# Kernel tuning notes

Hardware: AMD Instinct MI355X
Metric: run time of the kernel (lower is better)

The kernel has to match this reference:

```python
import jax, jax.numpy as jnp
import numpy as np

B, Te, Td, D_ENC, D_DEC, ATT = 8, 512, 128, 512, 512, 256


def setup_inputs() -> dict:
    key = jax.random.key(0)
    k0, k1, k2, k3, k4 = jax.random.split(key, 5)
    return {
        "values": jax.random.normal(k0, (B, Te, D_ENC), dtype=jnp.float32),
        "query": jax.random.normal(k1, (B, Td, D_DEC), dtype=jnp.float32),
        "W_h": jax.random.uniform(k2, (D_ENC, ATT), jnp.float32, -0.05, 0.05),
        "U_a": jax.random.uniform(k3, (D_DEC, ATT), jnp.float32, -0.05, 0.05),
        "V_a": jax.random.uniform(k4, (1, ATT), jnp.float32, -0.05, 0.05),
    }


def reference(values, query, W_h, U_a, V_a):
    # values: [B, Te, D_ENC] encoder output sequence (single entry in 'values' list)
    # query:  [B, Td, D_DEC] decoder output sequence
    # With a single encoder sequence, broadcast_sum/broadcast_concat reduces are identities.
    W_hi = jnp.einsum('bse,ea->bsa', values, W_h)        # [B, Te, ATT]
    U_a_dot_s = jnp.einsum('btd,da->bta', query, U_a)    # [B, Td, ATT]
    # tanh(h.Wa + s.Ua): vectorized over all decoder timesteps (K.rnn scan unrolled)
    act = jnp.tanh(W_hi[:, None, :, :] + U_a_dot_s[:, :, None, :])  # [B, Td, Te, ATT]
    scores = jnp.einsum('btsa,a->bts', act, V_a[0])      # [B, Td, Te]
    e_outputs = jax.nn.softmax(scores, axis=-1)          # softmax over encoder positions
    # context: weighted sum of encoder hidden states
    c_outputs = jnp.einsum('bts,bse->bte', e_outputs, values)  # [B, Td, D_ENC]
    return (c_outputs, e_outputs)
```

## Files before the change

kernel.cpp:

```cpp
#include <hip/hip_runtime.h>
#include <hip/hip_bf16.h>


typedef __attribute__((ext_vector_type(8))) short bf16x8;
typedef __attribute__((ext_vector_type(4))) float f32x4;

__device__ inline void f32_to_bf16_pair(float x, short& h, short& l) {
    unsigned u = __builtin_bit_cast(unsigned, x);
    unsigned r = u + 0x7FFFu + ((u >> 16) & 1u);
    h = (short)(r >> 16);
    float xh = __builtin_bit_cast(float, r & 0xFFFF0000u);
    float xl = x - xh;
    unsigned u2 = __builtin_bit_cast(unsigned, xl);
    unsigned r2 = u2 + 0x7FFFu + ((u2 >> 16) & 1u);
    l = (short)(r2 >> 16);
}

__global__ __launch_bounds__(256) void prep(
    const float* __restrict__ W_h, const float* __restrict__ U_a,
    const float* __restrict__ values, const float* __restrict__ query,
    short* __restrict__ BHi, short* __restrict__ BLo,
    short* __restrict__ AHi, short* __restrict__ ALo)
{
    __shared__ float TW[64][65];
    __shared__ float TA[16][516];
    const int bid = blockIdx.x;
    const int tid = threadIdx.x;

    if (bid < 64) {
        const int mat = bid >> 5, nb = (bid >> 3) & 3, kb = bid & 7;
        const float* W = mat ? U_a : W_h;
        {
            const int krow = tid >> 2, cq = (tid & 3) * 16;
            const float* src = W + (size_t)(kb * 64 + krow) * 256 + nb * 64 + cq;
            #pragma unroll
            for (int q = 0; q < 4; ++q)
                *(float4*)&TW[krow][cq + q * 4] = *(const float4*)&src[q * 4];
        }
        __syncthreads();
        {
            const int f = tid >> 5;
            const int ngl = f >> 1, ksl = f & 1;
            const int l0 = (tid & 31) * 2;
            const int ngrp = nb * 4 + ngl;
            const int ksg = kb * 2 + ksl;
            const size_t base = (size_t)mat * 131072 + (size_t)(ngrp * 16 + ksg) * 512;
            #pragma unroll
            for (int li = 0; li < 2; ++li) {
                const int lane = l0 + li;
                const int lr = lane & 15, lg = lane >> 4;
                bf16x8 hv, lv;
                #pragma unroll
                for (int j = 0; j < 8; ++j) {
                    short h, l;
                    f32_to_bf16_pair(TW[ksl * 32 + lg * 8 + j][ngl * 16 + lr], h, l);
                    hv[j] = h; lv[j] = l;
                }
                *(bf16x8*)(BHi + base + lane * 8) = hv;
                *(bf16x8*)(BLo + base + lane * 8) = lv;
            }
        }
    } else {
        const int mg = bid - 64;
        const float* src = (mg < 256) ? values + (size_t)mg * 16 * 512
                                      : query + (size_t)(mg - 256) * 16 * 512;
        {
            const int row = tid >> 4, c0 = (tid & 15) * 4;
            #pragma unroll
            for (int i = 0; i < 8; ++i)
                *(float4*)&TA[row][c0 + i * 64] =
                    *(const float4*)&src[(size_t)row * 512 + c0 + i * 64];
        }
        __syncthreads();
        {
            const int ks = tid >> 4;
            const int l4 = (tid & 15) * 4;
            const size_t base = ((size_t)(mg * 16 + ks)) * 512;
            #pragma unroll
            for (int li = 0; li < 4; ++li) {
                const int lane = l4 + li;
                const int lr = lane & 15, lg = lane >> 4;
                bf16x8 hv, lv;
                #pragma unroll
                for (int j = 0; j < 8; ++j) {
                    short h, l;
                    f32_to_bf16_pair(TA[lr][ks * 32 + lg * 8 + j], h, l);
                    hv[j] = h; lv[j] = l;
                }
                *(bf16x8*)(AHi + base + lane * 8) = hv;
                *(bf16x8*)(ALo + base + lane * 8) = lv;
            }
        }
    }
}

__global__ __launch_bounds__(128) void gemm_mfma(
    const short* __restrict__ AHi, const short* __restrict__ ALo,
    const short* __restrict__ BHi, const short* __restrict__ BLo,
    float* __restrict__ EwO, float* __restrict__ EuO)
{
    const int bid = blockIdx.x;
    const int mt = bid >> 2, nt = bid & 3;
    const int tid = threadIdx.x;
    const int w = tid >> 6, l = tid & 63;
    const int lr = l & 15, lg = l >> 4;

    float* C; int m0, mg, matoff;
    if (mt < 128) { C = EwO; m0 = mt * 32; mg = mt * 2 + w; matoff = 0; }
    else { C = EuO; m0 = (mt - 128) * 32; mg = 256 + (mt - 128) * 2 + w; matoff = 131072; }

    const short* ah_p = AHi + ((size_t)mg * 16) * 512 + l * 8;
    const short* al_p = ALo + ((size_t)mg * 16) * 512 + l * 8;
    const short* bh_p = BHi + matoff + ((size_t)(nt * 4) * 16) * 512 + l * 8;
    const short* bl_p = BLo + matoff + ((size_t)(nt * 4) * 16) * 512 + l * 8;

    f32x4 acc[4];
    #pragma unroll
    for (int nc = 0; nc < 4; ++nc) acc[nc] = (f32x4){0.f, 0.f, 0.f, 0.f};

    #pragma unroll 2
    for (int ks = 0; ks < 16; ++ks) {
        bf16x8 ah = *(const bf16x8*)(ah_p + (size_t)ks * 512);
        bf16x8 al = *(const bf16x8*)(al_p + (size_t)ks * 512);
        #pragma unroll
        for (int nc = 0; nc < 4; ++nc) {
            bf16x8 bh = *(const bf16x8*)(bh_p + ((size_t)(nc * 16 + ks)) * 512);
            bf16x8 bl = *(const bf16x8*)(bl_p + ((size_t)(nc * 16 + ks)) * 512);
            acc[nc] = __builtin_amdgcn_mfma_f32_16x16x32_bf16(ah, bh, acc[nc], 0, 0, 0);
            acc[nc] = __builtin_amdgcn_mfma_f32_16x16x32_bf16(al, bh, acc[nc], 0, 0, 0);
            acc[nc] = __builtin_amdgcn_mfma_f32_16x16x32_bf16(ah, bl, acc[nc], 0, 0, 0);
        }
    }

    const float SCL = 2.8853900817779268f;
    float* cp = C + (size_t)(m0 + w * 16 + lg * 4) * 256 + nt * 64 + lr;
    #pragma unroll
    for (int nc = 0; nc < 4; ++nc)
        #pragma unroll
        for (int r = 0; r < 4; ++r)
            cp[(size_t)r * 256 + nc * 16] = __builtin_amdgcn_exp2f(acc[nc][r] * SCL);
}

__global__ __launch_bounds__(256) void scores_k(
    const float* __restrict__ Ew, const float* __restrict__ Eu,
    const float* __restrict__ Va, float* __restrict__ scoresP)
{
    __shared__ float Ws[64][68];
    __shared__ float Us[16][68];

    const int bid = blockIdx.x;
    const int b = bid & 7;
    const int rest = bid >> 3;
    const int ah = rest & 3;
    const int tt = (rest >> 2) & 7;
    const int st = rest >> 5;
    const int t0 = tt * 16, s0 = st * 64, a0 = ah * 64;
    const int tid = threadIdx.x;

    const int r = tid >> 2, c16 = (tid & 3) * 16;
    const float* wsrc = Ew + (size_t)(b * 512 + s0 + r) * 256 + a0 + c16;
    #pragma unroll
    for (int q = 0; q < 4; ++q)
        *(float4*)&Ws[r][c16 + q * 4] = *(const float4*)&wsrc[q * 4];
    const int r8 = tid >> 4, c8 = (tid & 15) * 4;
    const float* usrc = Eu + (size_t)(b * 128 + t0 + r8) * 256 + a0 + c8;
    *(float4*)&Us[r8][c8] = *(const float4*)&usrc[0];
    __syncthreads();

    const int t = tid >> 4;
    const int ss = tid & 15;
    const float* Vp = Va + a0;

    float acc[4] = {};
    #pragma unroll 4
    for (int a = 0; a < 64; a += 4) {
        float4 u  = *(const float4*)&Us[t][a];
        float4 w0 = *(const float4*)&Ws[ss][a];
        float4 w1 = *(const float4*)&Ws[ss + 16][a];
        float4 w2 = *(const float4*)&Ws[ss + 32][a];
        float4 w3 = *(const float4*)&Ws[ss + 48][a];
        const float uv[4] = {u.x, u.y, u.z, u.w};
        const float wv[4][4] = {{w0.x, w0.y, w0.z, w0.w}, {w1.x, w1.y, w1.z, w1.w},
                                {w2.x, w2.y, w2.z, w2.w}, {w3.x, w3.y, w3.z, w3.w}};
        #pragma unroll
        for (int q = 0; q < 4; ++q) {
            const float vq = Vp[a + q];
            #pragma unroll
            for (int k = 0; k < 4; ++k) {
                float e = wv[k][q] * uv[q];
                float rc = __builtin_amdgcn_rcpf(1.f + e);
                acc[k] = fmaf(vq, rc, acc[k]);
            }
        }
    }

    float* sp = scoresP + (size_t)ah * 524288
              + (size_t)(b * 128 + t0 + t) * 512 + s0 + ss;
    #pragma unroll
    for (int k = 0; k < 4; ++k) sp[k * 16] = acc[k];
}

__global__ __launch_bounds__(256) void softctx(
    const float* __restrict__ scoresP, const float* __restrict__ values,
    float* __restrict__ out_c, float* __restrict__ out_e)
{
    __shared__ float Ps[4][512];
    __shared__ float Part[7][4][128];

    const int bid = blockIdx.x;
    const int b = bid & 7;
    const int rest = bid >> 3;
    const int tg = rest & 31;
    const int eh = rest >> 5;
    const int t0 = tg * 4;
    const int tid = threadIdx.x;

    {
        const int row = tid >> 6, lane = tid & 63;
        const float* sp = scoresP + (size_t)(b * 128 + t0 + row) * 512;
        float e[8]; float ssum = 0.f;
        #pragma unroll
        for (int k = 0; k < 8; ++k) {
            const int idx = k * 64 + lane;
            float s = sp[idx] + sp[524288 + idx] + sp[1048576 + idx] + sp[1572864 + idx];
            e[k] = __builtin_amdgcn_exp2f(s * -2.8853900817779268f);
            ssum += e[k];
        }
        #pragma unroll
        for (int off = 32; off > 0; off >>= 1)
            ssum += __shfl_xor(ssum, off);
        const float inv = 1.0f / ssum;
        float* erow = out_e + (size_t)(b * 128 + t0 + row) * 512;
        #pragma unroll
        for (int k = 0; k < 8; ++k) {
            float p = e[k] * inv;
            Ps[row][k * 64 + lane] = p;
            if (eh == 0) erow[k * 64 + lane] = p;
        }
    }
    __syncthreads();

    const int sh = tid >> 5;
    const int el = (tid & 31) * 4;
    const int e4 = eh * 128 + el;
    const int sb = sh * 64;
    const float* vb = values + (size_t)b * 262144;

    float4 a0 = {0,0,0,0}, a1 = {0,0,0,0}, a2 = {0,0,0,0}, a3 = {0,0,0,0};
    #pragma unroll 2
    for (int s2 = 0; s2 < 64; s2 += 4) {
        float4 q0 = *(const float4*)&Ps[0][sb + s2];
        float4 q1 = *(const float4*)&Ps[1][sb + s2];
        float4 q2 = *(const float4*)&Ps[2][sb + s2];
        float4 q3 = *(const float4*)&Ps[3][sb + s2];
        const float q0v[4] = {q0.x, q0.y, q0.z, q0.w};
        const float q1v[4] = {q1.x, q1.y, q1.z, q1.w};
        const float q2v[4] = {q2.x, q2.y, q2.z, q2.w};
        const float q3v[4] = {q3.x, q3.y, q3.z, q3.w};
        #pragma unroll
        for (int j = 0; j < 4; ++j) {
            float4 v4 = *(const float4*)&vb[(size_t)(sb + s2 + j) * 512 + e4];
            a0.x = fmaf(q0v[j], v4.x, a0.x); a0.y = fmaf(q0v[j], v4.y, a0.y);
            a0.z = fmaf(q0v[j], v4.z, a0.z); a0.w = fmaf(q0v[j], v4.w, a0.w);
            a1.x = fmaf(q1v[j], v4.x, a1.x); a1.y = fmaf(q1v[j], v4.y, a1.y);
            a1.z = fmaf(q1v[j], v4.z, a1.z); a1.w = fmaf(q1v[j], v4.w, a1.w);
            a2.x = fmaf(q2v[j], v4.x, a2.x); a2.y = fmaf(q2v[j], v4.y, a2.y);
            a2.z = fmaf(q2v[j], v4.z, a2.z); a2.w = fmaf(q2v[j], v4.w, a2.w);
            a3.x = fmaf(q3v[j], v4.x, a3.x); a3.y = fmaf(q3v[j], v4.y, a3.y);
            a3.z = fmaf(q3v[j], v4.z, a3.z); a3.w = fmaf(q3v[j], v4.w, a3.w);
        }
    }

    if (sh) {
        *(float4*)&Part[sh - 1][0][el] = a0;
        *(float4*)&Part[sh - 1][1][el] = a1;
        *(float4*)&Part[sh - 1][2][el] = a2;
        *(float4*)&Part[sh - 1][3][el] = a3;
    }
    __syncthreads();
    if (!sh) {
        #pragma unroll
        for (int rrow = 0; rrow < 4; ++rrow) {
            float4 acc = (rrow == 0) ? a0 : (rrow == 1) ? a1 : (rrow == 2) ? a2 : a3;
            #pragma unroll
            for (int g = 0; g < 7; ++g) {
                float4 p4 = *(const float4*)&Part[g][rrow][el];
                acc.x += p4.x; acc.y += p4.y; acc.z += p4.z; acc.w += p4.w;
            }
            *(float4*)&out_c[(size_t)(b * 128 + t0 + rrow) * 512 + e4] = acc;
        }
    }
}

extern "C" void kernel_launch(void* const* d_in, const int* in_sizes, int n_in,
                              void* d_out, int out_size, void* d_ws, size_t ws_size,
                              hipStream_t stream) {
    const float* values = (const float*)d_in[0];
    const float* query  = (const float*)d_in[1];
    const float* W_h    = (const float*)d_in[2];
    const float* U_a    = (const float*)d_in[3];
    const float* V_a    = (const float*)d_in[4];

    float* ws      = (float*)d_ws;
    float* Ew      = ws;
    float* Eu      = ws + 1048576;
    float* scoresP = ws + 1310720;
    short* S       = (short*)(ws + 3407872);
    short* AHi     = S;
    short* ALo     = S + 2621440;
    short* BHi     = S + 5242880;
    short* BLo     = S + 5505024;

    float* out_c = (float*)d_out;
    float* out_e = out_c + 8 * 128 * 512;

    hipLaunchKernelGGL(prep, dim3(384), dim3(256), 0, stream,
                       W_h, U_a, values, query, BHi, BLo, AHi, ALo);
    hipLaunchKernelGGL(gemm_mfma, dim3(640), dim3(128), 0, stream,
                       AHi, ALo, BHi, BLo, Ew, Eu);
    hipLaunchKernelGGL(scores_k, dim3(2048), dim3(256), 0, stream,
                       Ew, Eu, V_a, scoresP);
    hipLaunchKernelGGL(softctx, dim3(1024), dim3(256), 0, stream,
                       scoresP, values, out_c, out_e);
}
```

Baseline: 58.20 us.

## Fuse score computation with softmax and context into one kernel

```diff
diff --git a/kernel.cpp b/kernel.cpp
--- a/kernel.cpp
+++ b/kernel.cpp
@@ -141,125 +141,125 @@
             cp[(size_t)r * 256 + nc * 16] = __builtin_amdgcn_exp2f(acc[nc][r] * SCL);
 }
 
-__global__ __launch_bounds__(256) void scores_k(
+struct FA { float Ws[128][65]; float Us[4][260]; float Vs[256]; float red[8]; };
+struct FB { float Ps[4][512]; float Part[3][4][512]; };
+union FS { FA a; FB b; };
+
+__global__ __launch_bounds__(512, 1) void fused_sc(
     const float* __restrict__ Ew, const float* __restrict__ Eu,
-    const float* __restrict__ Va, float* __restrict__ scoresP)
+    const float* __restrict__ Va, const float* __restrict__ values,
+    float* __restrict__ out_c, float* __restrict__ out_e)
 {
-    __shared__ float Ws[64][68];
-    __shared__ float Us[16][68];
-
+    __shared__ FS sm;
     const int bid = blockIdx.x;
     const int b = bid & 7;
-    const int rest = bid >> 3;
-    const int ah = rest & 3;
-    const int tt = (rest >> 2) & 7;
-    const int st = rest >> 5;
-    const int t0 = tt * 16, s0 = st * 64, a0 = ah * 64;
+    const int t0 = (bid >> 3) * 4;
     const int tid = threadIdx.x;
-
-    const int r = tid >> 2, c16 = (tid & 3) * 16;
-    const float* wsrc = Ew + (size_t)(b * 512 + s0 + r) * 256 + a0 + c16;
+    const int w = tid >> 6;
+    const int t = w >> 1;
+    const int half = w & 1;
+    const int lane = tid & 63;
+    const int row = half * 64 + lane;
+
+    for (int k = tid; k < 1024; k += 512)
+        sm.a.Us[k >> 8][k & 255] =
+            Eu[(size_t)(b * 128 + t0 + (k >> 8)) * 256 + (k & 255)];
+    if (tid < 256) sm.a.Vs[tid] = Va[tid];
+
+    const int sr = tid >> 2;
+    const int scc = (tid & 3) * 16;
+    const float* ewb = Ew + (size_t)(b * 512) * 256;
+
+    float4 pre[4];
     #pragma unroll
     for (int q = 0; q < 4; ++q)
-        *(float4*)&Ws[r][c16 + q * 4] = *(const float4*)&wsrc[q * 4];
-    const int r8 = tid >> 4, c8 = (tid & 15) * 4;
-    const float* usrc = Eu + (size_t)(b * 128 + t0 + r8) * 256 + a0 + c8;
-    *(float4*)&Us[r8][c8] = *(const float4*)&usrc[0];
+        pre[q] = *(const float4*)&ewb[(size_t)sr * 256 + scc + q * 4];
+    #pragma unroll
+    for (int q = 0; q < 4; ++q)
+        *(float4*)&sm.a.Ws[sr][scc + q * 4] = pre[q];
     __syncthreads();
 
-    const int t = tid >> 4;
-    const int ss = tid & 15;
-    const float* Vp = Va + a0;
-
     float acc[4] = {};
-    #pragma unroll 4
-    for (int a = 0; a < 64; a += 4) {
-        float4 u  = *(const float4*)&Us[t][a];
-        float4 w0 = *(const float4*)&Ws[ss][a];
-        float4 w1 = *(const float4*)&Ws[ss + 16][a];
-        float4 w2 = *(const float4*)&Ws[ss + 32][a];
-        float4 w3 = *(const float4*)&Ws[ss + 48][a];
-        const float uv[4] = {u.x, u.y, u.z, u.w};
-        const float wv[4][4] = {{w0.x, w0.y, w0.z, w0.w}, {w1.x, w1.y, w1.z, w1.w},
-                                {w2.x, w2.y, w2.z, w2.w}, {w3.x, w3.y, w3.z, w3.w}};
-        #pragma unroll
-        for (int q = 0; q < 4; ++q) {
-            const float vq = Vp[a + q];
-            #pragma unroll
-            for (int k = 0; k < 4; ++k) {
-                float e = wv[k][q] * uv[q];
-                float rc = __builtin_amdgcn_rcpf(1.f + e);
-                acc[k] = fmaf(vq, rc, acc[k]);
-            }
-        }
-    }
-
-    float* sp = scoresP + (size_t)ah * 524288
-              + (size_t)(b * 128 + t0 + t) * 512 + s0 + ss;
-    #pragma unroll
-    for (int k = 0; k < 4; ++k) sp[k * 16] = acc[k];
-}
-
-__global__ __launch_bounds__(256) void softctx(
-    const float* __restrict__ scoresP, const float* __restrict__ values,
-    float* __restrict__ out_c, float* __restrict__ out_e)
-{
-    __shared__ float Ps[4][512];
-    __shared__ float Part[7][4][128];
-
-    const int bid = blockIdx.x;
-    const int b = bid & 7;
-    const int rest = bid >> 3;
-    const int tg = rest & 31;
-    const int eh = rest >> 5;
-    const int t0 = tg * 4;
-    const int tid = threadIdx.x;
-
-    {
-        const int row = tid >> 6, lane = tid & 63;
-        const float* sp = scoresP + (size_t)(b * 128 + t0 + row) * 512;
-        float e[8]; float ssum = 0.f;
-        #pragma unroll
-        for (int k = 0; k < 8; ++k) {
-            const int idx = k * 64 + lane;
-            float s = sp[idx] + sp[524288 + idx] + sp[1048576 + idx] + sp[1572864 + idx];
-            e[k] = __builtin_amdgcn_exp2f(s * -2.8853900817779268f);
-            ssum += e[k];
-        }
-        #pragma unroll
-        for (int off = 32; off > 0; off >>= 1)
-            ssum += __shfl_xor(ssum, off);
-        const float inv = 1.0f / ssum;
-        float* erow = out_e + (size_t)(b * 128 + t0 + row) * 512;
-        #pragma unroll
-        for (int k = 0; k < 8; ++k) {
-            float p = e[k] * inv;
-            Ps[row][k * 64 + lane] = p;
-            if (eh == 0) erow[k * 64 + lane] = p;
-        }
-    }
+    #pragma unroll
+    for (int i = 0; i < 16; ++i) {
+        const int sp = i >> 2, ac = i & 3;
+        if (i < 15) {
+            const int sp2 = (i + 1) >> 2, ac2 = (i + 1) & 3;
+            #pragma unroll
+            for (int q = 0; q < 4; ++q)
+                pre[q] = *(const float4*)&ewb[(size_t)(sp2 * 128 + sr) * 256
+                                              + ac2 * 64 + scc + q * 4];
+        }
+        float as = 0.f;
+        const float* wr = &sm.a.Ws[row][0];
+        const float* ur = &sm.a.Us[t][ac * 64];
+        const float* vr = &sm.a.Vs[ac * 64];
+        #pragma unroll 4
+        for (int a4 = 0; a4 < 16; ++a4) {
+            float4 wq = *(const float4*)&wr[a4 * 4];
+            float4 uq = *(const float4*)&ur[a4 * 4];
+            float4 vq = *(const float4*)&vr[a4 * 4];
+            float e0 = fmaf(wq.x, uq.x, 1.f);
+            float e1 = fmaf(wq.y, uq.y, 1.f);
+            float e2 = fmaf(wq.z, uq.z, 1.f);
+            float e3 = fmaf(wq.w, uq.w, 1.f);
+            as = fmaf(vq.x, __builtin_amdgcn_rcpf(e0), as);
+            as = fmaf(vq.y, __builtin_amdgcn_rcpf(e1), as);
+            as = fmaf(vq.z, __builtin_amdgcn_rcpf(e2), as);
+            as = fmaf(vq.w, __builtin_amdgcn_rcpf(e3), as);
+        }
+        acc[sp] += as;
+        __syncthreads();
+        if (i < 15) {
+            #pragma unroll
+            for (int q = 0; q < 4; ++q)
+                *(float4*)&sm.a.Ws[sr][scc + q * 4] = pre[q];
+            __syncthreads();
+        }
+    }
+
+    const float SCL = 2.8853900817779268f;
+    float ep[4]; float ssum = 0.f;
+    #pragma unroll
+    for (int sp = 0; sp < 4; ++sp) {
+        ep[sp] = __builtin_amdgcn_exp2f(acc[sp] * -SCL);
+        ssum += ep[sp];
+    }
+    #pragma unroll
+    for (int off = 32; off > 0; off >>= 1)
+        ssum += __shfl_xor(ssum, off);
+    if (lane == 0) sm.a.red[w] = ssum;
     __syncthreads();
-
-    const int sh = tid >> 5;
-    const int el = (tid & 31) * 4;
-    const int e4 = eh * 128 + el;
-    const int sb = sh * 64;
+    const float inv = 1.0f / (sm.a.red[t * 2] + sm.a.red[t * 2 + 1]);
+
+    float* erow = out_e + (size_t)(b * 128 + t0 + t) * 512;
+    #pragma unroll
+    for (int sp = 0; sp < 4; ++sp) {
+        float p = ep[sp] * inv;
+        sm.b.Ps[t][sp * 128 + row] = p;
+        erow[sp * 128 + row] = p;
+    }
+    __syncthreads();
+
+    const int sh = tid >> 7;
+    const int el = (tid & 127) * 4;
+    const int sb = sh * 128;
     const float* vb = values + (size_t)b * 262144;
 
     float4 a0 = {0,0,0,0}, a1 = {0,0,0,0}, a2 = {0,0,0,0}, a3 = {0,0,0,0};
     #pragma unroll 2
-    for (int s2 = 0; s2 < 64; s2 += 4) {
-        float4 q0 = *(const float4*)&Ps[0][sb + s2];
-        float4 q1 = *(const float4*)&Ps[1][sb + s2];
-        float4 q2 = *(const float4*)&Ps[2][sb + s2];
-        float4 q3 = *(const float4*)&Ps[3][sb + s2];
+    for (int s2 = 0; s2 < 128; s2 += 4) {
+        float4 q0 = *(const float4*)&sm.b.Ps[0][sb + s2];
+        float4 q1 = *(const float4*)&sm.b.Ps[1][sb + s2];
+        float4 q2 = *(const float4*)&sm.b.Ps[2][sb + s2];
+        float4 q3 = *(const float4*)&sm.b.Ps[3][sb + s2];
         const float q0v[4] = {q0.x, q0.y, q0.z, q0.w};
         const float q1v[4] = {q1.x, q1.y, q1.z, q1.w};
         const float q2v[4] = {q2.x, q2.y, q2.z, q2.w};
         const float q3v[4] = {q3.x, q3.y, q3.z, q3.w};
         #pragma unroll
         for (int j = 0; j < 4; ++j) {
-            float4 v4 = *(const float4*)&vb[(size_t)(sb + s2 + j) * 512 + e4];
+            float4 v4 = *(const float4*)&vb[(size_t)(sb + s2 + j) * 512 + el];
             a0.x = fmaf(q0v[j], v4.x, a0.x); a0.y = fmaf(q0v[j], v4.y, a0.y);
             a0.z = fmaf(q0v[j], v4.z, a0.z); a0.w = fmaf(q0v[j], v4.w, a0.w);
             a1.x = fmaf(q1v[j], v4.x, a1.x); a1.y = fmaf(q1v[j], v4.y, a1.y);
@@ -272,22 +272,22 @@
     }
 
     if (sh) {
-        *(float4*)&Part[sh - 1][0][el] = a0;
-        *(float4*)&Part[sh - 1][1][el] = a1;
-        *(float4*)&Part[sh - 1][2][el] = a2;
-        *(float4*)&Part[sh - 1][3][el] = a3;
+        *(float4*)&sm.b.Part[sh - 1][0][el] = a0;
+        *(float4*)&sm.b.Part[sh - 1][1][el] = a1;
+        *(float4*)&sm.b.Part[sh - 1][2][el] = a2;
+        *(float4*)&sm.b.Part[sh - 1][3][el] = a3;
     }
     __syncthreads();
     if (!sh) {
         #pragma unroll
         for (int rrow = 0; rrow < 4; ++rrow) {
-            float4 acc = (rrow == 0) ? a0 : (rrow == 1) ? a1 : (rrow == 2) ? a2 : a3;
-            #pragma unroll
-            for (int g = 0; g < 7; ++g) {
-                float4 p4 = *(const float4*)&Part[g][rrow][el];
-                acc.x += p4.x; acc.y += p4.y; acc.z += p4.z; acc.w += p4.w;
+            float4 accv = (rrow == 0) ? a0 : (rrow == 1) ? a1 : (rrow == 2) ? a2 : a3;
+            #pragma unroll
+            for (int g = 0; g < 3; ++g) {
+                float4 p4 = *(const float4*)&sm.b.Part[g][rrow][el];
+                accv.x += p4.x; accv.y += p4.y; accv.z += p4.z; accv.w += p4.w;
             }
-            *(float4*)&out_c[(size_t)(b * 128 + t0 + rrow) * 512 + e4] = acc;
+            *(float4*)&out_c[(size_t)(b * 128 + t0 + rrow) * 512 + el] = accv;
         }
     }
 }
@@ -304,7 +304,6 @@
     float* ws      = (float*)d_ws;
     float* Ew      = ws;
     float* Eu      = ws + 1048576;
-    float* scoresP = ws + 1310720;
     short* S       = (short*)(ws + 3407872);
     short* AHi     = S;
     short* ALo     = S + 2621440;
@@ -318,8 +317,6 @@
                        W_h, U_a, values, query, BHi, BLo, AHi, ALo);
     hipLaunchKernelGGL(gemm_mfma, dim3(640), dim3(128), 0, stream,
                        AHi, ALo, BHi, BLo, Ew, Eu);
-    hipLaunchKernelGGL(scores_k, dim3(2048), dim3(256), 0, stream,
-                       Ew, Eu, V_a, scoresP);
-    hipLaunchKernelGGL(softctx, dim3(1024), dim3(256), 0, stream,
-                       scoresP, values, out_c, out_e);
-}
+    hipLaunchKernelGGL(fused_sc, dim3(256), dim3(512), 0, stream,
+                       Ew, Eu, V_a, values, out_c, out_e);
+}
```

Result: slower. 124.4 us (+113.7%).
